# Kernel optimization log

Measured on AMD Instinct MI355X. Metric: run time of the kernel, lower is better.

## Reference

```python
import jax, jax.numpy as jnp
import numpy as np
from jax import lax

EPS = 1e-8
ROOT_2 = 1.41421
STYLE_SIZE = 512
OUT_CH = 512
STYLE_SCALE = (2.0 / STYLE_SIZE) ** 0.5   # Weight_Scaling(style_size): equalized-LR sqrt(2/fan_in)
OUT_SCALE = (2.0 / (OUT_CH * 1 * 1)) ** 0.5  # Weight_Scaling(out_channels*1*1)


def setup_inputs() -> dict:
    key = jax.random.key(0)
    ks = jax.random.split(key, 10)
    B, Cin, Cout, H, S = 8, 512, 512, 32, 512
    return {
        "x": jax.random.normal(ks[0], (B, Cin, H, H), dtype=jnp.float32),
        "style_base": jax.random.normal(ks[1], (B, S), dtype=jnp.float32),
        "noise": jax.random.normal(ks[2], (B, 1, 2 * H, 2 * H), dtype=jnp.float32),
        "t": jax.random.normal(ks[3], (B, Cout, 2 * H, 2 * H), dtype=jnp.float32),
        # learned params
        "affine_w": jax.random.normal(ks[4], (Cin, S), dtype=jnp.float32) * (1.0 / np.sqrt(S)),
        "affine_b": jnp.zeros((Cin,), dtype=jnp.float32),
        "conv_w": jax.random.normal(ks[5], (Cout, Cin, 3, 3), dtype=jnp.float32),
        "conv_b": jnp.zeros((1, Cout, 1, 1), dtype=jnp.float32),
        "prelu_a": jnp.asarray(0.25, dtype=jnp.float32),
        "noise_scalar": jnp.zeros((1, Cout, 1, 1), dtype=jnp.float32) + 0.1,
        "out_w": jax.random.normal(ks[6], (3, Cout, 1, 1), dtype=jnp.float32) * (1.0 / np.sqrt(Cout)),
        "out_b": jnp.zeros((3,), dtype=jnp.float32),
    }


def reference(x, style_base, noise, t, affine_w, affine_b, conv_w, conv_b,
              prelu_a, noise_scalar, out_w, out_b):
    B, Cin, H, W = x.shape
    # style_std = affine(Weight_Scaling(style_base)) + 1  -> [B, Cin]
    style_std = (style_base * STYLE_SCALE) @ affine_w.T + affine_b + 1.0

    # bilinear x2 upsample (align_corners=False == half-pixel, matches jax.image.resize)
    x = jax.image.resize(x, (B, Cin, 2 * H, 2 * W), method="bilinear")

    # modulated conv with L2 demodulation, expressed as input-scale + conv + output-scale
    # per-sample weight w_b[o,i,k,l] = w[o,i,k,l]*s[b,i] / ||w*s||_b,o
    wsq = jnp.sum(conv_w ** 2, axis=(2, 3))                      # [O, I]
    demod = 1.0 / jnp.sqrt(jnp.einsum("oi,bi->bo", wsq, style_std ** 2) + EPS)  # [B, O]
    xm = x * style_std[:, :, None, None]
    y = lax.conv_general_dilated(xm, conv_w, (1, 1), "SAME",
                                 dimension_numbers=("NCHW", "OIHW", "NCHW"))
    y = y * demod[:, :, None, None] + conv_b + noise_scalar * noise
    # PReLU (single shared slope)
    y = jnp.where(y >= 0, y, prelu_a * y)

    # out branch: skip add, scale, toRGB 1x1 conv, clamp
    y = (y + t) / ROOT_2
    out = lax.conv_general_dilated(y * OUT_SCALE, out_w, (1, 1), "SAME",
                                   dimension_numbers=("NCHW", "OIHW", "NCHW"))
    out = jnp.clip(out + out_b[None, :, None, None], 0.0, 1.0)
    return (y, out)
```

## Files before the change

kernel.cpp:

```cpp
#include <hip/hip_runtime.h>


typedef short bf16x8 __attribute__((ext_vector_type(8)));
typedef short short8v __attribute__((ext_vector_type(8)));
typedef float f32x16 __attribute__((ext_vector_type(16)));

#define WS_STYLE 0
#define WS_DEMOD 16384
#define WS_WSQ   32768
#define WS_WPACK 1081344
#define WS_XM    5799936
#define WS_PART  41484288

__device__ __forceinline__ short f2bf(float f) {
  unsigned u = __float_as_uint(f);
  u += 0x7FFFu + ((u >> 16) & 1u);
  return (short)(u >> 16);
}

__device__ __forceinline__ void gld16(const short* g, char* l) {
  __builtin_amdgcn_global_load_lds((const __attribute__((address_space(1))) void*)g,
                                   (__attribute__((address_space(3))) void*)l,
                                   16, 0, 0);
}

__global__ void k_style(const float* __restrict__ sb, const float* __restrict__ aw,
                        const float* __restrict__ ab, float* __restrict__ style) {
  __shared__ float s_sb[512];
  int b = blockIdx.x;
  for (int i = threadIdx.x; i < 512; i += 256) s_sb[i] = sb[b * 512 + i] * 0.0625f;
  __syncthreads();
  for (int i = threadIdx.x; i < 512; i += 256) {
    const float4* wrow = (const float4*)(aw + (size_t)i * 512);
    float acc = 0.f;
    #pragma unroll 4
    for (int s4 = 0; s4 < 128; ++s4) {
      float4 w4 = wrow[s4];
      float4 sv = *(const float4*)(s_sb + s4 * 4);
      acc += w4.x * sv.x + w4.y * sv.y + w4.z * sv.z + w4.w * sv.w;
    }
    style[b * 512 + i] = acc + ab[i] + 1.0f;
  }
}

__global__ void k_wsq(const float* __restrict__ cw, float* __restrict__ wsq) {
  int idx = blockIdx.x * 256 + threadIdx.x;
  const float* p = cw + (size_t)idx * 9;
  float s = 0.f;
  #pragma unroll
  for (int j = 0; j < 9; ++j) s += p[j] * p[j];
  wsq[idx] = s;
}

__global__ void k_demod(const float* __restrict__ wsq, const float* __restrict__ style,
                        float* __restrict__ demod) {
  int wid = threadIdx.x >> 6, lane = threadIdx.x & 63;
  int idx = blockIdx.x * 4 + wid;
  int b = idx >> 9, o = idx & 511;
  const float* wr = wsq + (size_t)o * 512;
  const float* ss = style + b * 512;
  float sum = 0.f;
  #pragma unroll
  for (int k = 0; k < 8; ++k) {
    int i = k * 64 + lane;
    float s = ss[i];
    sum += wr[i] * s * s;
  }
  #pragma unroll
  for (int off = 32; off; off >>= 1) sum += __shfl_down(sum, off);
  if (lane == 0) demod[b * 512 + o] = rsqrtf(sum + 1e-8f);
}

__global__ void k_upsample(const float* __restrict__ x, const float* __restrict__ style,
                           short* __restrict__ xm) {
  int b = blockIdx.x / 66, hp = blockIdx.x % 66;
  short* xmp = xm + ((size_t)b * 66 + hp) * 66 * 512;
  if (hp == 0 || hp == 65) {
    short8v z = {0, 0, 0, 0, 0, 0, 0, 0};
    for (int u = threadIdx.x; u < 66 * 512 / 8; u += 256) ((short8v*)xmp)[u] = z;
    return;
  }
  int h = hp - 1;
  int j0 = (h >> 1) - 1 + (h & 1);
  float fj = (h & 1) ? 0.25f : 0.75f;
  int j0c = j0 < 0 ? 0 : j0;
  int j1c = j0 + 1 > 31 ? 31 : j0 + 1;
  __shared__ float xt[2][64][33];
  int ccc = threadIdx.x & 63;
  int wsub = threadIdx.x >> 6;
  for (int c0 = 0; c0 < 512; c0 += 64) {
    __syncthreads();
    #pragma unroll 4
    for (int k = 0; k < 16; ++k) {
      int idx = k * 256 + threadIdx.x;
      int ii = idx & 31, cc = (idx >> 5) & 63, jj = idx >> 11;
      xt[jj][cc][ii] = x[(((size_t)b * 512 + c0 + cc) * 32 + (jj ? j1c : j0c)) * 32 + ii];
    }
    __syncthreads();
    float sstyle = style[b * 512 + c0 + ccc];
    #pragma unroll 4
    for (int wk = 0; wk < 16; ++wk) {
      int w = wk * 4 + wsub;
      int i0 = (w >> 1) - 1 + (w & 1);
      float fi = (w & 1) ? 0.25f : 0.75f;
      int i0c = i0 < 0 ? 0 : i0;
      int i1c = i0 + 1 > 31 ? 31 : i0 + 1;
      float v0 = xt[0][ccc][i0c] * (1.f - fi) + xt[0][ccc][i1c] * fi;
      float v1 = xt[1][ccc][i0c] * (1.f - fi) + xt[1][ccc][i1c] * fi;
      float v = (v0 * (1.f - fj) + v1 * fj) * sstyle;
      xmp[(size_t)(w + 1) * 512 + c0 + ccc] = f2bf(v);
    }
    if (wsub == 0) {
      xmp[c0 + ccc] = 0;
      xmp[(size_t)65 * 512 + c0 + ccc] = 0;
    }
  }
}

__global__ void k_packw(const float* __restrict__ cw, short* __restrict__ wpk) {
  int unit = blockIdx.x * 256 + threadIdx.x;
  int s = unit >> 11;
  int rem = unit & 2047;
  int o = rem >> 2, sp = rem & 3;
  int tap = s >> 4, cc = s & 15;
  int i0 = cc * 32 + ((sp ^ ((o >> 1) & 3)) << 3);
  const float* src = cw + ((size_t)o * 512 + i0) * 9 + tap;
  short8v v;
  #pragma unroll
  for (int j = 0; j < 8; ++j) v[j] = f2bf(src[j * 9]);
  *(short8v*)(wpk + (size_t)unit * 8) = v;
}

__global__ __launch_bounds__(512, 2) void k_conv(
    const short* __restrict__ xm, const short* __restrict__ wpk,
    const float* __restrict__ demod, const float* __restrict__ convb,
    const float* __restrict__ nscal, const float* __restrict__ noise,
    const float* __restrict__ t, const float* __restrict__ prelu_a,
    const float* __restrict__ ow, float* __restrict__ part,
    float* __restrict__ y) {
  __shared__ char WTs[2][49152];
  __shared__ char XMs[2][25344];

  int tid = threadIdx.x;
  int bid = blockIdx.x;
  int cohalf = bid & 1, hq = (bid >> 1) & 15, b = bid >> 5;
  int wid = tid >> 6, lane = tid & 63;
  int wo = wid & 1, wsrow = wid >> 1;
  int l31 = lane & 31, lg = lane >> 5;

  const short* xb = xm + ((size_t)b * 66 + hq * 4) * 66 * 512;
  const short* wpkh = wpk + (size_t)cohalf * 256 * 32;
  int wb0 = ((wo * 128 + l31) << 6) + ((lg ^ ((l31 >> 1) & 3)) << 4);

  #pragma unroll
  for (int k = 0; k < 3; ++k) {
    int u = k * 512 + tid;
    int r = u / 264, rem = u - r * 264;
    int wp = rem >> 2, sp = rem & 3;
    gld16(xb + (size_t)(r * 66 + wp) * 512 + ((sp ^ ((wp >> 1) & 3)) << 3), XMs[0] + u * 16);
  }
  if (tid < 48) {
    int u = 1536 + tid;
    int rem = u - 1320;
    int wp = rem >> 2, sp = rem & 3;
    gld16(xb + (size_t)(5 * 66 + wp) * 512 + ((sp ^ ((wp >> 1) & 3)) << 3), XMs[0] + u * 16);
  }
  #pragma unroll
  for (int j = 0; j < 3; ++j) {
    const short* ws = wpkh + (size_t)(j * 16) * 16384;
    gld16(ws + tid * 8, WTs[0] + j * 16384 + tid * 16);
    gld16(ws + (512 + tid) * 8, WTs[0] + j * 16384 + (512 + tid) * 16);
  }

  f32x16 zf = {0,0,0,0,0,0,0,0,0,0,0,0,0,0,0,0};
  f32x16 acc[4][2];
  #pragma unroll
  for (int i = 0; i < 4; ++i) { acc[i][0] = zf; acc[i][1] = zf; }

  asm volatile("s_waitcnt vmcnt(0)" ::: "memory");
  __builtin_amdgcn_s_barrier();
  __builtin_amdgcn_sched_barrier(0);

  #pragma unroll 1
  for (int cc = 0; cc < 16; ++cc) {
    const char* XMc = (const char*)XMs[cc & 1];
    char* XMn = (char*)XMs[(cc & 1) ^ 1];
    #pragma unroll
    for (int krow = 0; krow < 3; ++krow) {
      int g = cc * 3 + krow;
      const char* WTc = (const char*)WTs[g & 1];
      char* WTn = (char*)WTs[(g & 1) ^ 1];

      if (g < 47) {
        int nkrow = (krow < 2) ? krow + 1 : 0;
        int ncc = (krow < 2) ? cc : cc + 1;
        #pragma unroll
        for (int j = 0; j < 3; ++j) {
          const short* ws = wpkh + (size_t)((nkrow * 3 + j) * 16 + ncc) * 16384;
          gld16(ws + tid * 8, WTn + j * 16384 + tid * 16);
          gld16(ws + (512 + tid) * 8, WTn + j * 16384 + (512 + tid) * 16);
        }
      }
      if (krow == 0 && cc < 15) {
        const short* xs = xb + (cc + 1) * 32;
        #pragma unroll
        for (int k = 0; k < 3; ++k) {
          int u = k * 512 + tid;
          int r = u / 264, rem = u - r * 264;
          int wp = rem >> 2, sp = rem & 3;
          gld16(xs + (size_t)(r * 66 + wp) * 512 + ((sp ^ ((wp >> 1) & 3)) << 3), XMn + u * 16);
        }
        if (tid < 48) {
          int u = 1536 + tid;
          int rem = u - 1320;
          int wp = rem >> 2, sp = rem & 3;
          gld16(xs + (size_t)(5 * 66 + wp) * 512 + ((sp ^ ((wp >> 1) & 3)) << 3), XMn + u * 16);
        }
      }

      #pragma unroll
      for (int j = 0; j < 3; ++j) {
        const char* Wp = WTc + j * 16384;
        bf16x8 wf0[4], wf1[4];
        #pragma unroll
        for (int cf = 0; cf < 4; ++cf) {
          wf0[cf] = *(const bf16x8*)(Wp + (wb0 + cf * 2048));
          wf1[cf] = *(const bf16x8*)(Wp + ((wb0 + cf * 2048) ^ 32));
        }
        int a = l31 + j;
        int xo = ((wsrow + krow) * 66 + a) * 64 + ((lg ^ ((a >> 1) & 3)) << 4);
        bf16x8 xf00 = *(const bf16x8*)(XMc + xo);
        bf16x8 xf01 = *(const bf16x8*)(XMc + xo + 2048);
        bf16x8 xf10 = *(const bf16x8*)(XMc + (xo ^ 32));
        bf16x8 xf11 = *(const bf16x8*)(XMc + ((xo ^ 32) + 2048));

        #pragma unroll
        for (int cf = 0; cf < 4; ++cf) {
          acc[cf][0] = __builtin_amdgcn_mfma_f32_32x32x16_bf16(wf0[cf], xf00, acc[cf][0], 0, 0, 0);
          acc[cf][1] = __builtin_amdgcn_mfma_f32_32x32x16_bf16(wf0[cf], xf01, acc[cf][1], 0, 0, 0);
        }
        #pragma unroll
        for (int cf = 0; cf < 4; ++cf) {
          acc[cf][0] = __builtin_amdgcn_mfma_f32_32x32x16_bf16(wf1[cf], xf10, acc[cf][0], 0, 0, 0);
          acc[cf][1] = __builtin_amdgcn_mfma_f32_32x32x16_bf16(wf1[cf], xf11, acc[cf][1], 0, 0, 0);
        }
      }

      asm volatile("s_waitcnt vmcnt(0)" ::: "memory");
      __builtin_amdgcn_s_barrier();
      __builtin_amdgcn_sched_barrier(0);
    }
  }

  float pa = prelu_a[0];
  const float inv_r2 = 1.0f / 1.41421f;
  int h = hq * 4 + wsrow;
  float nz0 = noise[((size_t)b * 64 + h) * 64 + l31];
  float nz1 = noise[((size_t)b * 64 + h) * 64 + 32 + l31];
  float pr[3][2] = {{0.f, 0.f}, {0.f, 0.f}, {0.f, 0.f}};
  #pragma unroll
  for (int cf = 0; cf < 4; ++cf) {
    #pragma unroll
    for (int reg = 0; reg < 16; ++reg) {
      int orow = (reg & 3) + 8 * (reg >> 2) + 4 * lg;
      int o = cohalf * 256 + wo * 128 + cf * 32 + orow;
      float dm = demod[b * 512 + o];
      float cb = convb[o];
      float ns = nscal[o];
      float w0 = ow[o], w1 = ow[512 + o], w2 = ow[1024 + o];
      #pragma unroll
      for (int sf = 0; sf < 2; ++sf) {
        int w = sf * 32 + l31;
        float v = acc[cf][sf][reg];
        v = v * dm + cb + ns * (sf ? nz1 : nz0);
        v = (v >= 0.f) ? v : pa * v;
        size_t oi = (((size_t)b * 512 + o) * 64 + h) * 64 + w;
        v = (v + t[oi]) * inv_r2;
        y[oi] = v;
        pr[0][sf] += v * w0;
        pr[1][sf] += v * w1;
        pr[2][sf] += v * w2;
      }
    }
  }
  #pragma unroll
  for (int c = 0; c < 3; ++c) {
    #pragma unroll
    for (int sf = 0; sf < 2; ++sf)
      pr[c][sf] += __shfl_down(pr[c][sf], 32);
  }
  if (lane < 32) {
    int slice = cohalf * 2 + wo;
    float* pp = part + (((size_t)(slice * 8 + b) * 3) * 64 + h) * 64;
    #pragma unroll
    for (int c = 0; c < 3; ++c) {
      #pragma unroll
      for (int sf = 0; sf < 2; ++sf)
        pp[(size_t)c * 4096 + sf * 32 + l31] = pr[c][sf];
    }
  }
}

__global__ void k_rgbfin(const float* __restrict__ part, const float* __restrict__ ob,
                         float* __restrict__ out) {
  int idx = blockIdx.x * 256 + threadIdx.x;
  int c = (idx / 4096) % 3;
  float s = part[idx] + part[98304 + idx] + part[196608 + idx] + part[294912 + idx];
  s = s * 0.0625f + ob[c];
  s = fminf(fmaxf(s, 0.f), 1.f);
  out[idx] = s;
}

extern "C" void kernel_launch(void* const* d_in, const int* in_sizes, int n_in,
                              void* d_out, int out_size, void* d_ws, size_t ws_size,
                              hipStream_t stream) {
  const float* x     = (const float*)d_in[0];
  const float* sb    = (const float*)d_in[1];
  const float* noise = (const float*)d_in[2];
  const float* t     = (const float*)d_in[3];
  const float* aw    = (const float*)d_in[4];
  const float* ab    = (const float*)d_in[5];
  const float* cw    = (const float*)d_in[6];
  const float* cb    = (const float*)d_in[7];
  const float* pa    = (const float*)d_in[8];
  const float* ns    = (const float*)d_in[9];
  const float* ow    = (const float*)d_in[10];
  const float* ob    = (const float*)d_in[11];
  char* ws = (char*)d_ws;
  float* style = (float*)(ws + WS_STYLE);
  float* demod = (float*)(ws + WS_DEMOD);
  float* wsq   = (float*)(ws + WS_WSQ);
  short* wpk   = (short*)(ws + WS_WPACK);
  short* xmw   = (short*)(ws + WS_XM);
  float* part  = (float*)(ws + WS_PART);
  float* y   = (float*)d_out;
  float* out = y + 16777216;

  k_style<<<8, 256, 0, stream>>>(sb, aw, ab, style);
  k_wsq<<<1024, 256, 0, stream>>>(cw, wsq);
  k_demod<<<1024, 256, 0, stream>>>(wsq, style, demod);
  k_upsample<<<528, 256, 0, stream>>>(x, style, xmw);
  k_packw<<<1152, 256, 0, stream>>>(cw, wpk);
  k_conv<<<256, 512, 0, stream>>>(xmw, wpk, demod, cb, ns, noise, t, pa, ow, part, y);
  k_rgbfin<<<384, 256, 0, stream>>>(part, ob, out);
}
```

Before: 220.8 us.

## Split conv blocks into output-channel quarters and stage activations through registers

The conv kernel now launches 512 blocks of 256 threads, each handling 128 output channels instead of 256. Shared memory shrinks to a smaller weight double buffer and a single activation buffer, which should let more blocks fit per CU. Activation tiles for the next input-channel chunk are prefetched into registers during the last kernel-row step and written to LDS after a barrier. The cost is an extra barrier and more register pressure, and each activation tile is now reloaded by twice as many blocks.

```diff
diff --git a/kernel.cpp b/kernel.cpp
--- a/kernel.cpp
+++ b/kernel.cpp
@@ -131,45 +131,59 @@
   *(short8v*)(wpk + (size_t)unit * 8) = v;
 }
 
-__global__ __launch_bounds__(512, 2) void k_conv(
+__global__ __launch_bounds__(256, 2) void k_conv(
     const short* __restrict__ xm, const short* __restrict__ wpk,
     const float* __restrict__ demod, const float* __restrict__ convb,
     const float* __restrict__ nscal, const float* __restrict__ noise,
     const float* __restrict__ t, const float* __restrict__ prelu_a,
     const float* __restrict__ ow, float* __restrict__ part,
     float* __restrict__ y) {
-  __shared__ char WTs[2][49152];
-  __shared__ char XMs[2][25344];
+  __shared__ char WTs[6][8192];
+  __shared__ char XMb[25344];
 
   int tid = threadIdx.x;
   int bid = blockIdx.x;
-  int cohalf = bid & 1, hq = (bid >> 1) & 15, b = bid >> 5;
-  int wid = tid >> 6, lane = tid & 63;
-  int wo = wid & 1, wsrow = wid >> 1;
+  int coq = bid & 3, hq = (bid >> 2) & 15, b = bid >> 6;
+  int wsrow = tid >> 6, lane = tid & 63;
   int l31 = lane & 31, lg = lane >> 5;
 
   const short* xb = xm + ((size_t)b * 66 + hq * 4) * 66 * 512;
-  const short* wpkh = wpk + (size_t)cohalf * 256 * 32;
-  int wb0 = ((wo * 128 + l31) << 6) + ((lg ^ ((l31 >> 1) & 3)) << 4);
-
-  #pragma unroll
-  for (int k = 0; k < 3; ++k) {
-    int u = k * 512 + tid;
-    int r = u / 264, rem = u - r * 264;
-    int wp = rem >> 2, sp = rem & 3;
-    gld16(xb + (size_t)(r * 66 + wp) * 512 + ((sp ^ ((wp >> 1) & 3)) << 3), XMs[0] + u * 16);
-  }
-  if (tid < 48) {
-    int u = 1536 + tid;
-    int rem = u - 1320;
-    int wp = rem >> 2, sp = rem & 3;
-    gld16(xb + (size_t)(5 * 66 + wp) * 512 + ((sp ^ ((wp >> 1) & 3)) << 3), XMs[0] + u * 16);
-  }
+  const short* wpkq = wpk + (size_t)coq * 128 * 32;
+  int wb0 = (l31 << 6) + ((lg ^ ((l31 >> 1) & 3)) << 4);
+
+  int off0, off1, off2, off3, off4, off5, off6;
+  int d0, d1, d2, d3, d4, d5, d6;
+  {
+    int u, r, rem, wp, sp;
+    u = tid;        r = u / 264; rem = u - r * 264; wp = rem >> 2; sp = rem & 3;
+    off0 = (r * 66 + wp) * 512 + ((sp ^ ((wp >> 1) & 3)) << 3); d0 = u * 16;
+    u = 256 + tid;  r = u / 264; rem = u - r * 264; wp = rem >> 2; sp = rem & 3;
+    off1 = (r * 66 + wp) * 512 + ((sp ^ ((wp >> 1) & 3)) << 3); d1 = u * 16;
+    u = 512 + tid;  r = u / 264; rem = u - r * 264; wp = rem >> 2; sp = rem & 3;
+    off2 = (r * 66 + wp) * 512 + ((sp ^ ((wp >> 1) & 3)) << 3); d2 = u * 16;
+    u = 768 + tid;  r = u / 264; rem = u - r * 264; wp = rem >> 2; sp = rem & 3;
+    off3 = (r * 66 + wp) * 512 + ((sp ^ ((wp >> 1) & 3)) << 3); d3 = u * 16;
+    u = 1024 + tid; r = u / 264; rem = u - r * 264; wp = rem >> 2; sp = rem & 3;
+    off4 = (r * 66 + wp) * 512 + ((sp ^ ((wp >> 1) & 3)) << 3); d4 = u * 16;
+    u = 1280 + tid; r = u / 264; rem = u - r * 264; wp = rem >> 2; sp = rem & 3;
+    off5 = (r * 66 + wp) * 512 + ((sp ^ ((wp >> 1) & 3)) << 3); d5 = u * 16;
+    u = 1536 + (tid & 63); if (u > 1583) u = 1583;
+    r = u / 264; rem = u - r * 264; wp = rem >> 2; sp = rem & 3;
+    off6 = (r * 66 + wp) * 512 + ((sp ^ ((wp >> 1) & 3)) << 3); d6 = u * 16;
+  }
+
+  gld16(xb + off0, XMb + d0);
+  gld16(xb + off1, XMb + d1);
+  gld16(xb + off2, XMb + d2);
+  gld16(xb + off3, XMb + d3);
+  gld16(xb + off4, XMb + d4);
+  gld16(xb + off5, XMb + d5);
+  if (tid < 48) gld16(xb + off6, XMb + d6);
   #pragma unroll
   for (int j = 0; j < 3; ++j) {
-    const short* ws = wpkh + (size_t)(j * 16) * 16384;
-    gld16(ws + tid * 8, WTs[0] + j * 16384 + tid * 16);
-    gld16(ws + (512 + tid) * 8, WTs[0] + j * 16384 + (512 + tid) * 16);
+    const short* ws = wpkq + (size_t)(j * 16) * 16384;
+    gld16(ws + tid * 8, WTs[j] + tid * 16);
+    gld16(ws + (256 + tid) * 8, WTs[j] + (256 + tid) * 16);
   }
 
   f32x16 zf = {0,0,0,0,0,0,0,0,0,0,0,0,0,0,0,0};
@@ -181,46 +195,40 @@
   __builtin_amdgcn_s_barrier();
   __builtin_amdgcn_sched_barrier(0);
 
+  short8v xr0, xr1, xr2, xr3, xr4, xr5, xr6;
+
   #pragma unroll 1
   for (int cc = 0; cc < 16; ++cc) {
-    const char* XMc = (const char*)XMs[cc & 1];
-    char* XMn = (char*)XMs[(cc & 1) ^ 1];
     #pragma unroll
     for (int krow = 0; krow < 3; ++krow) {
       int g = cc * 3 + krow;
-      const char* WTc = (const char*)WTs[g & 1];
-      char* WTn = (char*)WTs[(g & 1) ^ 1];
+      const char* WTc = (const char*)WTs + (size_t)((g & 1) * 3) * 8192;
+      char* WTn = (char*)WTs + (size_t)(((g + 1) & 1) * 3) * 8192;
 
       if (g < 47) {
         int nkrow = (krow < 2) ? krow + 1 : 0;
         int ncc = (krow < 2) ? cc : cc + 1;
         #pragma unroll
         for (int j = 0; j < 3; ++j) {
-          const short* ws = wpkh + (size_t)((nkrow * 3 + j) * 16 + ncc) * 16384;
-          gld16(ws + tid * 8, WTn + j * 16384 + tid * 16);
-          gld16(ws + (512 + tid) * 8, WTn + j * 16384 + (512 + tid) * 16);
-        }
-      }
-      if (krow == 0 && cc < 15) {
+          const short* ws = wpkq + (size_t)((nkrow * 3 + j) * 16 + ncc) * 16384;
+          gld16(ws + tid * 8, WTn + j * 8192 + tid * 16);
+          gld16(ws + (256 + tid) * 8, WTn + j * 8192 + (256 + tid) * 16);
+        }
+      }
+      if (krow == 2 && cc < 15) {
         const short* xs = xb + (cc + 1) * 32;
-        #pragma unroll
-        for (int k = 0; k < 3; ++k) {
-          int u = k * 512 + tid;
-          int r = u / 264, rem = u - r * 264;
-          int wp = rem >> 2, sp = rem & 3;
-          gld16(xs + (size_t)(r * 66 + wp) * 512 + ((sp ^ ((wp >> 1) & 3)) << 3), XMn + u * 16);
-        }
-        if (tid < 48) {
-          int u = 1536 + tid;
-          int rem = u - 1320;
-          int wp = rem >> 2, sp = rem & 3;
-          gld16(xs + (size_t)(5 * 66 + wp) * 512 + ((sp ^ ((wp >> 1) & 3)) << 3), XMn + u * 16);
-        }
+        xr0 = *(const short8v*)(xs + off0);
+        xr1 = *(const short8v*)(xs + off1);
+        xr2 = *(const short8v*)(xs + off2);
+        xr3 = *(const short8v*)(xs + off3);
+        xr4 = *(const short8v*)(xs + off4);
+        xr5 = *(const short8v*)(xs + off5);
+        if (tid < 48) xr6 = *(const short8v*)(xs + off6);
       }
 
       #pragma unroll
       for (int j = 0; j < 3; ++j) {
-        const char* Wp = WTc + j * 16384;
+        const char* Wp = WTc + j * 8192;
         bf16x8 wf0[4], wf1[4];
         #pragma unroll
         for (int cf = 0; cf < 4; ++cf) {
@@ -229,10 +237,10 @@
         }
         int a = l31 + j;
         int xo = ((wsrow + krow) * 66 + a) * 64 + ((lg ^ ((a >> 1) & 3)) << 4);
-        bf16x8 xf00 = *(const bf16x8*)(XMc + xo);
-        bf16x8 xf01 = *(const bf16x8*)(XMc + xo + 2048);
-        bf16x8 xf10 = *(const bf16x8*)(XMc + (xo ^ 32));
-        bf16x8 xf11 = *(const bf16x8*)(XMc + ((xo ^ 32) + 2048));
+        bf16x8 xf00 = *(const bf16x8*)(XMb + xo);
+        bf16x8 xf01 = *(const bf16x8*)(XMb + xo + 2048);
+        bf16x8 xf10 = *(const bf16x8*)(XMb + (xo ^ 32));
+        bf16x8 xf11 = *(const bf16x8*)(XMb + ((xo ^ 32) + 2048));
 
         #pragma unroll
         for (int cf = 0; cf < 4; ++cf) {
@@ -246,9 +254,26 @@
         }
       }
 
-      asm volatile("s_waitcnt vmcnt(0)" ::: "memory");
-      __builtin_amdgcn_s_barrier();
-      __builtin_amdgcn_sched_barrier(0);
+      if (krow < 2) {
+        asm volatile("s_waitcnt vmcnt(0)" ::: "memory");
+        __builtin_amdgcn_s_barrier();
+        __builtin_amdgcn_sched_barrier(0);
+      } else {
+        asm volatile("s_waitcnt vmcnt(0) lgkmcnt(0)" ::: "memory");
+        __builtin_amdgcn_s_barrier();
+        if (cc < 15) {
+          *(short8v*)(XMb + d0) = xr0;
+          *(short8v*)(XMb + d1) = xr1;
+          *(short8v*)(XMb + d2) = xr2;
+          *(short8v*)(XMb + d3) = xr3;
+          *(short8v*)(XMb + d4) = xr4;
+          *(short8v*)(XMb + d5) = xr5;
+          if (tid < 48) *(short8v*)(XMb + d6) = xr6;
+        }
+        asm volatile("s_waitcnt lgkmcnt(0)" ::: "memory");
+        __builtin_amdgcn_s_barrier();
+        __builtin_amdgcn_sched_barrier(0);
+      }
     }
   }
 
@@ -263,7 +288,7 @@
     #pragma unroll
     for (int reg = 0; reg < 16; ++reg) {
       int orow = (reg & 3) + 8 * (reg >> 2) + 4 * lg;
-      int o = cohalf * 256 + wo * 128 + cf * 32 + orow;
+      int o = coq * 128 + cf * 32 + orow;
       float dm = demod[b * 512 + o];
       float cb = convb[o];
       float ns = nscal[o];
@@ -290,7 +315,7 @@
       pr[c][sf] += __shfl_down(pr[c][sf], 32);
   }
   if (lane < 32) {
-    int slice = cohalf * 2 + wo;
+    int slice = coq;
     float* pp = part + (((size_t)(slice * 8 + b) * 3) * 64 + h) * 64;
     #pragma unroll
     for (int c = 0; c < 3; ++c) {
@@ -341,6 +366,6 @@
   k_demod<<<1024, 256, 0, stream>>>(wsq, style, demod);
   k_upsample<<<528, 256, 0, stream>>>(x, style, xmw);
   k_packw<<<1152, 256, 0, stream>>>(cw, wpk);
-  k_conv<<<256, 512, 0, stream>>>(xmw, wpk, demod, cb, ns, noise, t, pa, ow, part, y);
+  k_conv<<<512, 256, 0, stream>>>(xmw, wpk, demod, cb, ns, noise, t, pa, ow, part, y);
   k_rgbfin<<<384, 256, 0, stream>>>(part, ob, out);
 }
```

Result: no change. 218.5 us (-1.0%).
